# Kernel optimization log

Hardware: AMD Instinct MI355X
Metric: run time of the kernel (lower is better)

Reference implementation:

```python
import jax, jax.numpy as jnp
import numpy as np

N, E, HID, ED, L, H, D = 65536, 262144, 256, 64, 2, 8, 32
FF = 4 * HID
A_START = 8192  # first action gripper node; nodes [A_START:] are the T*K action nodes


def _ln(x, s, b, eps=1e-5):
    mu = jnp.mean(x, -1, keepdims=True)
    var = jnp.var(x, -1, keepdims=True)
    return (x - mu) * jax.lax.rsqrt(var + eps) * s + b


def _gnn_forward(x, edge_attr, edge_index, Wq, Wk, Wv, WeK, WeV, Wo,
                 ln1_s, ln1_b, ffn_w1, ffn_b1, ffn_w2, ffn_b2, ln2_s, ln2_b):
    # Hetero graph transformer over the single ('gripper','action','gripper') relation:
    # per-layer edge-indexed gather -> multi-head attention with edge features ->
    # segment softmax over incoming edges -> scatter-aggregate -> residual/LN/FFN.
    n = x.shape[0]
    e = edge_attr.shape[0]
    src, dst = edge_index[0], edge_index[1]
    inv_sqrt_d = np.float32(1.0 / np.sqrt(D))
    for l in range(Wq.shape[0]):
        q = (x @ Wq[l]).reshape(n, H, D)
        k = (x @ Wk[l]).reshape(n, H, D)
        v = (x @ Wv[l]).reshape(n, H, D)
        kj = k[src] + (edge_attr @ WeK[l]).reshape(e, H, D)  # [E,H,D] gathered keys + edge bias
        vj = v[src] + (edge_attr @ WeV[l]).reshape(e, H, D)
        score = jnp.einsum('ehd,ehd->eh', q[dst], kj) * inv_sqrt_d  # [E,H]
        smax = jax.ops.segment_max(score, dst, num_segments=n)
        p = jnp.exp(score - smax[dst])
        denom = jax.ops.segment_sum(p, dst, num_segments=n)
        alpha = p / denom[dst]  # segment softmax over incoming edges
        agg = jax.ops.segment_sum((alpha[..., None] * vj).reshape(e, H * D), dst, num_segments=n)
        x = _ln(x + agg @ Wo[l], ln1_s[l], ln1_b[l])
        hid = jax.nn.gelu(x @ ffn_w1[l] + ffn_b1[l], approximate=False) @ ffn_w2[l] + ffn_b2[l]
        x = _ln(x + hid, ln2_s[l], ln2_b[l])
    return x


def setup_inputs() -> dict:
    key = jax.random.key(0)
    ks = iter(jax.random.split(key, 16))
    w = lambda shape: jax.random.normal(next(ks), shape, jnp.float32) * 0.05
    return {
        "all_gripper_feats": jax.random.normal(next(ks), (N, HID), jnp.float32),
        "edge_attr": jax.random.normal(next(ks), (E, ED), jnp.float32),
        "Wq": w((L, HID, H * D)), "Wk": w((L, HID, H * D)), "Wv": w((L, HID, H * D)),
        "WeK": w((L, ED, H * D)), "WeV": w((L, ED, H * D)), "Wo": w((L, H * D, HID)),
        "ln1_s": jnp.ones((L, HID), jnp.float32), "ln1_b": jnp.zeros((L, HID), jnp.float32),
        "ffn_w1": w((L, HID, FF)), "ffn_b1": jnp.zeros((L, FF), jnp.float32),
        "ffn_w2": w((L, FF, HID)), "ffn_b2": jnp.zeros((L, HID), jnp.float32),
        "ln2_s": jnp.ones((L, HID), jnp.float32), "ln2_b": jnp.zeros((L, HID), jnp.float32),
        "head_w1": w((HID, HID)), "head_b1": jnp.zeros((HID,), jnp.float32),
        "head_w2": w((HID, 7)), "head_b2": jnp.zeros((7,), jnp.float32),
        "edge_index": jax.random.randint(next(ks), (2, E), 0, N),
        "action_start": A_START,
    }


def reference(all_gripper_feats, edge_attr, Wq, Wk, Wv, WeK, WeV, Wo,
              ln1_s, ln1_b, ffn_w1, ffn_b1, ffn_w2, ffn_b2, ln2_s, ln2_b,
              head_w1, head_b1, head_w2, head_b2, edge_index, action_start):
    x = _gnn_forward(all_gripper_feats, edge_attr, edge_index, Wq, Wk, Wv, WeK, WeV, Wo,
                     ln1_s, ln1_b, ffn_w1, ffn_b1, ffn_w2, ffn_b2, ln2_s, ln2_b)
    a = x[action_start:]  # action gripper nodes (T*K, hidden)
    return jax.nn.gelu(a @ head_w1 + head_b1, approximate=False) @ head_w2 + head_b2  # (T*K, 7)
```

## Files before the change

kernel.cpp:

```cpp
#include <hip/hip_runtime.h>
#include <hip/hip_bf16.h>
#include <math.h>

#define NN     65536
#define NE     262144
#define HIDN   256
#define EDIM   64
#define NHEAD  8
#define FFN    1024
#define ASTART 8192
#define NACT   (NN - ASTART)
#define NCH    32768
#define NCHUNK (NE / NCH)
#define DPC    (NN / NCHUNK)
#define RCH    32768

typedef __attribute__((ext_vector_type(8))) short short8;
typedef __attribute__((ext_vector_type(4))) short short4v;
typedef __attribute__((ext_vector_type(4))) float float4v;
typedef __hip_bfloat16 bf16;

__device__ __forceinline__ float b2f(short s) {
    union { unsigned u; float f; } c;
    c.u = ((unsigned)(unsigned short)s) << 16;
    return c.f;
}
__device__ __forceinline__ short f2b(float f) {
    __hip_bfloat16 h = __float2bfloat16(f);
    return *reinterpret_cast<short*>(&h);
}
__device__ __forceinline__ float gelu_exact(float v) {
    return 0.5f * v * (1.0f + erff(v * 0.70710678118654752f));
}
__device__ __forceinline__ void gload16(const void* g, void* l) {
    __builtin_amdgcn_global_load_lds(
        (const __attribute__((address_space(1))) void*)(uintptr_t)g,
        (__attribute__((address_space(3))) void*)(unsigned)(uintptr_t)l,
        16, 0, 0);
}

__global__ void convert_kernel(const float* __restrict__ src,
                               bf16* __restrict__ dst, int n) {
    int i = blockIdx.x * 256 + threadIdx.x;
    if (i < n) dst[i] = __float2bfloat16(src[i]);
}

__global__ void transpose_kernel(const float* __restrict__ src,
                                 bf16* __restrict__ dst, int R, int Cc) {
    int idx = blockIdx.x * 256 + threadIdx.x;
    if (idx >= R * Cc) return;
    int r = idx / Cc, c = idx - r * Cc;
    dst[(size_t)c * R + r] = __float2bfloat16(src[idx]);
}

__global__ void hist_kernel(const int* __restrict__ dstI, int* __restrict__ cnt) {
    int i = blockIdx.x * 256 + threadIdx.x;
    if (i < NE) atomicAdd(&cnt[dstI[i]], 1);
}
__global__ void scan1_kernel(const int* __restrict__ cnt, int* __restrict__ rp,
                             int* __restrict__ bsum) {
    __shared__ int s[256];
    int t = threadIdx.x, i = blockIdx.x * 256 + t;
    int v = cnt[i]; s[t] = v; __syncthreads();
    for (int off = 1; off < 256; off <<= 1) {
        int x = (t >= off) ? s[t - off] : 0; __syncthreads();
        s[t] += x; __syncthreads();
    }
    rp[i] = s[t] - v;
    if (t == 255) bsum[blockIdx.x] = s[255];
}
__global__ void scan2_kernel(int* __restrict__ bsum) {
    __shared__ int s[256];
    int t = threadIdx.x; int v = bsum[t]; s[t] = v; __syncthreads();
    for (int off = 1; off < 256; off <<= 1) {
        int x = (t >= off) ? s[t - off] : 0; __syncthreads();
        s[t] += x; __syncthreads();
    }
    bsum[t] = s[t] - v;
}
__global__ void scan3_kernel(int* __restrict__ rp, const int* __restrict__ bsum,
                             int* __restrict__ cursor) {
    int i = blockIdx.x * 256 + threadIdx.x;
    int v = rp[i] + bsum[i >> 8];
    rp[i] = v; cursor[i] = v;
    if (i == 0) rp[NN] = NE;
}
__global__ void scatter_kernel(const int* __restrict__ srcI, const int* __restrict__ dstI,
                               int* __restrict__ cursor, int* __restrict__ perm,
                               int* __restrict__ src_s, int* __restrict__ dst_s) {
    int e = blockIdx.x * 256 + threadIdx.x;
    if (e >= NE) return;
    int d = dstI[e];
    int pos = atomicAdd(&cursor[d], 1);
    perm[pos] = e; src_s[pos] = srcI[e]; dst_s[pos] = d;
}

template<int AMODE, bool DO_GELU>
__global__ __launch_bounds__(256) void gemm_kernel(
    const void* __restrict__ A,
    const bf16* __restrict__ BT,
    const bf16* __restrict__ bias,
    bf16* __restrict__ C,
    int M, int Nn, int K,
    const int* __restrict__ perm)
{
    __shared__ __align__(16) short As[2][128 * 32];
    __shared__ __align__(16) short Bs[2][128 * 32];

    const int t    = threadIdx.x;
    const int wave = t >> 6;
    const int lane = t & 63;
    const int l15  = lane & 15;
    const int quad = lane >> 4;
    const int wm   = (wave & 1) * 64;
    const int wn   = (wave >> 1) * 64;
    const int bm   = blockIdx.y * 128;
    const int bn   = blockIdx.x * 128;
    const int srow = t >> 2;
    const int sw   = srow & 3;
    const int scolB = ((t & 3) ^ sw) * 8;
    const int scolA = (t & 3) * 8;

    const short* Ab = (const short*)A  + (size_t)(bm + srow) * K + scolB;
    const short* Bb = (const short*)BT + (size_t)(bn + srow) * K + scolB;
    const float* Af0 = nullptr;
    const float* Af1 = nullptr;
    if (AMODE == 1) {
        Af0 = (const float*)A + (size_t)(bm + srow) * K + scolA;
        Af1 = Af0 + (size_t)64 * K;
    } else if (AMODE == 2) {
        const int pr0 = perm[bm + srow];
        const int pr1 = perm[bm + 64 + srow];
        Af0 = (const float*)A + (size_t)pr0 * K + scolA;
        Af1 = (const float*)A + (size_t)pr1 * K + scolA;
    }
    const int offW  = wave * 1024;
    const int offTs = (t * 16) ^ (sw << 4);
    const int qs16  = (quad ^ (l15 & 3)) * 16;

    float4v acc[4][4];
    #pragma unroll
    for (int i = 0; i < 4; ++i)
        #pragma unroll
        for (int j = 0; j < 4; ++j) acc[i][j] = (float4v){0.f, 0.f, 0.f, 0.f};

    const int nt = K >> 5;

    auto STAGE = [&](int b, int k0) {
        char* lA = (char*)As[b];
        char* lB = (char*)Bs[b];
        if (AMODE == 0) {
            gload16(Ab + k0,                  lA + offW);
            gload16(Ab + (size_t)64 * K + k0, lA + 4096 + offW);
        } else {
            #pragma unroll
            for (int i = 0; i < 2; ++i) {
                const float* s = (i ? Af1 : Af0) + k0;
                float4v f0 = *(const float4v*)s;
                float4v f1 = *(const float4v*)(s + 4);
                short8 w;
                #pragma unroll
                for (int j = 0; j < 4; ++j) { w[j] = f2b(f0[j]); w[4 + j] = f2b(f1[j]); }
                *(short8*)(lA + i * 4096 + offTs) = w;
            }
        }
        gload16(Bb + k0,                  lB + offW);
        gload16(Bb + (size_t)64 * K + k0, lB + 4096 + offW);
    };

    STAGE(0, 0);
    __syncthreads();

    for (int kt = 0; kt < nt; ++kt) {
        const int cur = kt & 1;
        if (kt + 1 < nt) STAGE(cur ^ 1, (kt + 1) * 32);

        const char* lA = (const char*)As[cur];
        const char* lB = (const char*)Bs[cur];
        short8 afr[4], bfr[4];
        #pragma unroll
        for (int i = 0; i < 4; ++i)
            afr[i] = *(const short8*)(lA + (wm + i * 16 + l15) * 64 + qs16);
        #pragma unroll
        for (int j = 0; j < 4; ++j)
            bfr[j] = *(const short8*)(lB + (wn + j * 16 + l15) * 64 + qs16);
        #pragma unroll
        for (int i = 0; i < 4; ++i)
            #pragma unroll
            for (int j = 0; j < 4; ++j)
                acc[i][j] = __builtin_amdgcn_mfma_f32_16x16x32_bf16(afr[i], bfr[j], acc[i][j], 0, 0, 0);
        __syncthreads();
    }

    #pragma unroll
    for (int j = 0; j < 4; ++j) {
        const int col = bn + wn + j * 16 + l15;
        const float bv = bias ? b2f(((const short*)bias)[col]) : 0.0f;
        #pragma unroll
        for (int i = 0; i < 4; ++i) {
            const int row0 = bm + wm + i * 16 + quad * 4;
            #pragma unroll
            for (int r = 0; r < 4; ++r) {
                float v = acc[i][j][r] + bv;
                if (DO_GELU) v = gelu_exact(v);
                C[(size_t)(row0 + r) * Nn + col] = __float2bfloat16(v);
            }
        }
    }
}

__global__ __launch_bounds__(256) void score_kernel(
    const bf16* __restrict__ q, const bf16* __restrict__ k,
    const bf16* __restrict__ eK,
    const int* __restrict__ src_s, const int* __restrict__ dst_s,
    short* __restrict__ pbuf, int e0, int qkstride)
{
    const int p = e0 + blockIdx.x * 4 + (threadIdx.x >> 6);
    const int lane = threadIdx.x & 63;
    const int s = src_s[p], d = dst_s[p];
    const int off = lane * 4;

    const short4v qv = *(const short4v*)((const short*)q  + (size_t)d * qkstride + off);
    const short4v kv = *(const short4v*)((const short*)k  + (size_t)s * qkstride + off);
    const short4v ev = *(const short4v*)((const short*)eK + (size_t)(p - e0) * HIDN + off);
    float x = 0.f;
    #pragma unroll
    for (int j = 0; j < 4; ++j) x += b2f(qv[j]) * (b2f(kv[j]) + b2f(ev[j]));
    x += __shfl_xor(x, 1);
    x += __shfl_xor(x, 2);
    x += __shfl_xor(x, 4);
    if ((lane & 7) == 0) {
        const float sc = fminf(fmaxf(x * 0.17677669529663689f, -30.f), 30.f);
        pbuf[(size_t)p * NHEAD + (lane >> 3)] = f2b(expf(sc));
    }
}

__global__ __launch_bounds__(256) void agg_kernel(
    const short* __restrict__ pbuf, const bf16* __restrict__ v,
    const bf16* __restrict__ eV,
    const int* __restrict__ src_s, const int* __restrict__ rp,
    float* __restrict__ agg, int e0, int e1, int dlo)
{
    const int d = dlo + blockIdx.x * 4 + (threadIdx.x >> 6);
    const int lane = threadIdx.x & 63;
    const int es = rp[d], ee = rp[d + 1];
    const int lo = es > e0 ? es : e0;
    const int hi = ee < e1 ? ee : e1;
    if (lo >= hi) return;
    const int h = lane >> 3, off = lane * 4;

    float den = 0.f;
    for (int p = es; p < ee; ++p) den += b2f(pbuf[(size_t)p * NHEAD + h]);

    float a0 = 0.f, a1 = 0.f, a2 = 0.f, a3 = 0.f;
    for (int p = lo; p < hi; ++p) {
        const float al = b2f(pbuf[(size_t)p * NHEAD + h]) / den;
        const int s = src_s[p];
        const short4v vv = *(const short4v*)((const short*)v  + (size_t)s * HIDN + off);
        const short4v ev = *(const short4v*)((const short*)eV + (size_t)(p - e0) * HIDN + off);
        a0 += al * (b2f(vv[0]) + b2f(ev[0]));
        a1 += al * (b2f(vv[1]) + b2f(ev[1]));
        a2 += al * (b2f(vv[2]) + b2f(ev[2]));
        a3 += al * (b2f(vv[3]) + b2f(ev[3]));
    }
    float* ao = agg + (size_t)d * HIDN + off;
    if (es >= e0 && ee <= e1) {
        *(float4v*)ao = (float4v){a0, a1, a2, a3};
    } else {
        atomicAdd(ao + 0, a0); atomicAdd(ao + 1, a1);
        atomicAdd(ao + 2, a2); atomicAdd(ao + 3, a3);
    }
}

__global__ __launch_bounds__(256) void ln_kernel(
    bf16* __restrict__ x, const bf16* __restrict__ t,
    const bf16* __restrict__ sc, const bf16* __restrict__ bi, int r0)
{
    const int row = r0 + blockIdx.x * 4 + (threadIdx.x >> 6);
    const int lane = threadIdx.x & 63;
    const size_t base = (size_t)row * HIDN + lane * 4;
    const size_t tbase = (size_t)(row - r0) * HIDN + lane * 4;
    const short4v xv = *(const short4v*)((const short*)x + base);
    const short4v tv = *(const short4v*)((const short*)t + tbase);
    float v[4];
    #pragma unroll
    for (int j = 0; j < 4; ++j) v[j] = b2f(xv[j]) + b2f(tv[j]);
    float sum = v[0] + v[1] + v[2] + v[3];
    float ssq = v[0]*v[0] + v[1]*v[1] + v[2]*v[2] + v[3]*v[3];
    #pragma unroll
    for (int m = 1; m < 64; m <<= 1) { sum += __shfl_xor(sum, m); ssq += __shfl_xor(ssq, m); }
    const float mean = sum * (1.0f / 256.0f);
    const float var  = fmaxf(ssq * (1.0f / 256.0f) - mean * mean, 0.0f);
    const float rstd = rsqrtf(var + 1e-5f);
    const short4v sv = *(const short4v*)((const short*)sc + lane * 4);
    const short4v bv = *(const short4v*)((const short*)bi + lane * 4);
    short4v out;
    #pragma unroll
    for (int j = 0; j < 4; ++j)
        out[j] = f2b((v[j] - mean) * rstd * b2f(sv[j]) + b2f(bv[j]));
    *(short4v*)((short*)x + base) = out;
}

__global__ __launch_bounds__(256) void head2_kernel(
    const bf16* __restrict__ h1, const bf16* __restrict__ w2T,
    const bf16* __restrict__ b2, float* __restrict__ out)
{
    const int row = blockIdx.x * 4 + (threadIdx.x >> 6);
    const int lane = threadIdx.x & 63;
    const int off = lane * 4;
    const short4v hv = *(const short4v*)((const short*)h1 + (size_t)row * HIDN + off);
    float hf[4];
    #pragma unroll
    for (int j = 0; j < 4; ++j) hf[j] = b2f(hv[j]);
    float acc[7];
    #pragma unroll
    for (int jc = 0; jc < 7; ++jc) {
        const short4v wv = *(const short4v*)((const short*)w2T + jc * HIDN + off);
        float a = hf[0]*b2f(wv[0]) + hf[1]*b2f(wv[1]) + hf[2]*b2f(wv[2]) + hf[3]*b2f(wv[3]);
        #pragma unroll
        for (int m = 1; m < 64; m <<= 1) a += __shfl_xor(a, m);
        acc[jc] = a;
    }
    if (lane < 7) {
        float r = lane == 0 ? acc[0] : lane == 1 ? acc[1] : lane == 2 ? acc[2] :
                  lane == 3 ? acc[3] : lane == 4 ? acc[4] : lane == 5 ? acc[5] : acc[6];
        out[(size_t)row * 7 + lane] = r + b2f(((const short*)b2)[lane]);
    }
}

extern "C" void kernel_launch(void* const* d_in, const int* in_sizes, int n_in,
                              void* d_out, int out_size, void* d_ws, size_t ws_size,
                              hipStream_t stream)
{
    const float* xin   = (const float*)d_in[0];
    const float* eattr = (const float*)d_in[1];
    const float* Wq    = (const float*)d_in[2];
    const float* Wk    = (const float*)d_in[3];
    const float* Wv    = (const float*)d_in[4];
    const float* WeK   = (const float*)d_in[5];
    const float* WeV   = (const float*)d_in[6];
    const float* Wo    = (const float*)d_in[7];
    const float* ln1s  = (const float*)d_in[8];
    const float* ln1b  = (const float*)d_in[9];
    const float* fw1   = (const float*)d_in[10];
    const float* fb1   = (const float*)d_in[11];
    const float* fw2   = (const float*)d_in[12];
    const float* fb2   = (const float*)d_in[13];
    const float* ln2s  = (const float*)d_in[14];
    const float* ln2b  = (const float*)d_in[15];
    const float* hw1   = (const float*)d_in[16];
    const float* hb1   = (const float*)d_in[17];
    const float* hw2   = (const float*)d_in[18];
    const float* hb2   = (const float*)d_in[19];
    const int*  eidx   = (const int*)d_in[20];
    const int*  srcI   = eidx;
    const int*  dstI   = eidx + NE;

    char* base = (char*)d_ws;
    size_t off = 0;
    auto carve = [&](size_t bytes) -> char* {
        char* p = base + off;
        off += (bytes + 255) & ~(size_t)255;
        return p;
    };
    bf16*  x_b    = (bf16*) carve((size_t)NN * HIDN * 2);
    bf16*  qk_b   = (bf16*) carve((size_t)NN * 2 * HIDN * 2);
    bf16*  v_b    = (bf16*) carve((size_t)NN * HIDN * 2);
    bf16*  echunk = (bf16*) carve((size_t)NCH * HIDN * 2);
    short* pbuf   = (short*)carve((size_t)NE * NHEAD * 2);
    int*   perm   = (int*)  carve((size_t)NE * 4);
    int*   src_s  = (int*)  carve((size_t)NE * 4);
    int*   dst_s  = (int*)  carve((size_t)NE * 4);
    int*   rowp   = (int*)  carve((size_t)(NN + 1) * 4);
    bf16*  WqkT   = (bf16*) carve((size_t)2 * HIDN * HIDN * 2);
    bf16*  WvT    = (bf16*) carve((size_t)HIDN * HIDN * 2);
    bf16*  WoT    = (bf16*) carve((size_t)HIDN * HIDN * 2);
    bf16*  WeKT   = (bf16*) carve((size_t)HIDN * EDIM * 2);
    bf16*  WeVT   = (bf16*) carve((size_t)HIDN * EDIM * 2);
    bf16*  W1T    = (bf16*) carve((size_t)FFN * HIDN * 2);
    bf16*  W2T    = (bf16*) carve((size_t)HIDN * FFN * 2);
    bf16*  HW1T   = (bf16*) carve((size_t)HIDN * HIDN * 2);
    bf16*  HW2T   = (bf16*) carve((size_t)8 * HIDN * 2);
    bf16*  c_ln1s = (bf16*) carve((size_t)2 * HIDN * 2);
    bf16*  c_ln1b = (bf16*) carve((size_t)2 * HIDN * 2);
    bf16*  c_ln2s = (bf16*) carve((size_t)2 * HIDN * 2);
    bf16*  c_ln2b = (bf16*) carve((size_t)2 * HIDN * 2);
    bf16*  c_fb1  = (bf16*) carve((size_t)2 * FFN * 2);
    bf16*  c_fb2  = (bf16*) carve((size_t)2 * HIDN * 2);
    bf16*  c_hb1  = (bf16*) carve((size_t)HIDN * 2);
    bf16*  c_hb2  = (bf16*) carve((size_t)16 * 2);
    if (off > ws_size) return;

    int* cnt    = (int*)echunk;
    int* cursor = cnt + NN;
    int* bsum   = cursor + NN;
    float* agg    = (float*)qk_b;
    bf16*  tmp_b  = v_b;
    bf16*  hid    = qk_b;
    bf16*  ffnout = v_b;

    const int TB = 256;
    #define GRID1(n) dim3(((n) + TB - 1) / TB)

    convert_kernel<<<GRID1(NN * HIDN), TB, 0, stream>>>(xin, x_b, NN * HIDN);
    convert_kernel<<<GRID1(2 * HIDN), TB, 0, stream>>>(ln1s, c_ln1s, 2 * HIDN);
    convert_kernel<<<GRID1(2 * HIDN), TB, 0, stream>>>(ln1b, c_ln1b, 2 * HIDN);
    convert_kernel<<<GRID1(2 * HIDN), TB, 0, stream>>>(ln2s, c_ln2s, 2 * HIDN);
    convert_kernel<<<GRID1(2 * HIDN), TB, 0, stream>>>(ln2b, c_ln2b, 2 * HIDN);
    convert_kernel<<<GRID1(2 * FFN), TB, 0, stream>>>(fb1, c_fb1, 2 * FFN);
    convert_kernel<<<GRID1(2 * HIDN), TB, 0, stream>>>(fb2, c_fb2, 2 * HIDN);
    convert_kernel<<<GRID1(HIDN), TB, 0, stream>>>(hb1, c_hb1, HIDN);
    convert_kernel<<<1, TB, 0, stream>>>(hb2, c_hb2, 7);
    transpose_kernel<<<GRID1(HIDN * HIDN), TB, 0, stream>>>(hw1, HW1T, HIDN, HIDN);
    transpose_kernel<<<GRID1(HIDN * 7), TB, 0, stream>>>(hw2, HW2T, HIDN, 7);

    hipMemsetAsync(cnt, 0, (size_t)NN * 4, stream);
    hist_kernel<<<GRID1(NE), TB, 0, stream>>>(dstI, cnt);
    scan1_kernel<<<NN / 256, 256, 0, stream>>>(cnt, rowp, bsum);
    scan2_kernel<<<1, 256, 0, stream>>>(bsum);
    scan3_kernel<<<NN / 256, 256, 0, stream>>>(rowp, bsum, cursor);
    scatter_kernel<<<GRID1(NE), TB, 0, stream>>>(srcI, dstI, cursor, perm, src_s, dst_s);

    for (int l = 0; l < 2; ++l) {
        transpose_kernel<<<GRID1(HIDN * HIDN), TB, 0, stream>>>(Wq + (size_t)l*HIDN*HIDN, WqkT, HIDN, HIDN);
        transpose_kernel<<<GRID1(HIDN * HIDN), TB, 0, stream>>>(Wk + (size_t)l*HIDN*HIDN, WqkT + (size_t)HIDN*HIDN, HIDN, HIDN);
        transpose_kernel<<<GRID1(HIDN * HIDN), TB, 0, stream>>>(Wv + (size_t)l*HIDN*HIDN, WvT, HIDN, HIDN);
        transpose_kernel<<<GRID1(EDIM * HIDN), TB, 0, stream>>>(WeK + (size_t)l*EDIM*HIDN, WeKT, EDIM, HIDN);
        transpose_kernel<<<GRID1(EDIM * HIDN), TB, 0, stream>>>(WeV + (size_t)l*EDIM*HIDN, WeVT, EDIM, HIDN);
        transpose_kernel<<<GRID1(HIDN * HIDN), TB, 0, stream>>>(Wo + (size_t)l*HIDN*HIDN, WoT, HIDN, HIDN);
        transpose_kernel<<<GRID1(HIDN * FFN),  TB, 0, stream>>>(fw1 + (size_t)l*HIDN*FFN, W1T, HIDN, FFN);
        transpose_kernel<<<GRID1(FFN * HIDN),  TB, 0, stream>>>(fw2 + (size_t)l*FFN*HIDN, W2T, FFN, HIDN);

        gemm_kernel<0, false><<<dim3((2*HIDN)/128, NN/128), TB, 0, stream>>>(x_b, WqkT, nullptr, qk_b, NN, 2*HIDN, HIDN, nullptr);
        gemm_kernel<0, false><<<dim3(HIDN/128, NN/128), TB, 0, stream>>>(x_b, WvT, nullptr, v_b, NN, HIDN, HIDN, nullptr);

        for (int c = 0; c < NCHUNK; ++c) {
            gemm_kernel<2, false><<<dim3(HIDN/128, NCH/128), TB, 0, stream>>>(
                eattr, WeKT, nullptr, echunk, NCH, HIDN, EDIM, perm + (size_t)c * NCH);
            score_kernel<<<NCH / 4, TB, 0, stream>>>(qk_b, qk_b + HIDN, echunk, src_s, dst_s, pbuf, c * NCH, 2 * HIDN);
        }

        hipMemsetAsync(agg, 0, (size_t)NN * HIDN * 4, stream);
        for (int c = 0; c < NCHUNK; ++c) {
            gemm_kernel<2, false><<<dim3(HIDN/128, NCH/128), TB, 0, stream>>>(
                eattr, WeVT, nullptr, echunk, NCH, HIDN, EDIM, perm + (size_t)c * NCH);
            const int dlo = (c == 0) ? 0 : (c - 1) * DPC;
            const int dhi = (c == NCHUNK - 1) ? NN : (c + 2) * DPC;
            agg_kernel<<<(dhi - dlo) / 4, TB, 0, stream>>>(
                pbuf, v_b, echunk, src_s, rowp, agg, c * NCH, (c + 1) * NCH, dlo);
        }

        gemm_kernel<1, false><<<dim3(HIDN/128, NN/128), TB, 0, stream>>>(agg, WoT, nullptr, tmp_b, NN, HIDN, HIDN, nullptr);
        ln_kernel<<<NN / 4, TB, 0, stream>>>(x_b, tmp_b, c_ln1s + (size_t)l * HIDN, c_ln1b + (size_t)l * HIDN, 0);

        for (int r0 = 0; r0 < NN; r0 += RCH) {
            gemm_kernel<0, true ><<<dim3(FFN/128, RCH/128), TB, 0, stream>>>(
                x_b + (size_t)r0 * HIDN, W1T, c_fb1 + (size_t)l * FFN, hid, RCH, FFN, HIDN, nullptr);
            gemm_kernel<0, false><<<dim3(HIDN/128, RCH/128), TB, 0, stream>>>(
                hid, W2T, c_fb2 + (size_t)l * HIDN, ffnout, RCH, HIDN, FFN, nullptr);
            ln_kernel<<<RCH / 4, TB, 0, stream>>>(x_b, ffnout, c_ln2s + (size_t)l * HIDN, c_ln2b + (size_t)l * HIDN, r0);
        }
    }

    gemm_kernel<0, true><<<dim3(HIDN/128, NACT/128), TB, 0, stream>>>(
        x_b + (size_t)ASTART * HIDN, HW1T, c_hb1, hid, NACT, HIDN, HIDN, nullptr);
    head2_kernel<<<NACT / 4, TB, 0, stream>>>(hid, HW2T, c_hb2, (float*)d_out);
}
```

Baseline: 1.704 ms.

## Approximate GELU, remap GEMM blocks across XCDs, vectorize input conversion

Three separate changes. The exact erff-based GELU in the GEMM epilogue becomes an Abramowitz-Stegun polynomial erf built on a hardware reciprocal and fast exp. The GEMM block index is remapped so neighbouring tiles land on the same XCD, for better L2 reuse. The large fp32-to-bf16 input conversion now handles four elements per thread with vector loads and stores. The erf approximation has about 1e-7 absolute error, which bf16 output hides, but it is a numeric change.

```diff
diff --git a/kernel.cpp b/kernel.cpp
--- a/kernel.cpp
+++ b/kernel.cpp
@@ -29,8 +29,16 @@
     __hip_bfloat16 h = __float2bfloat16(f);
     return *reinterpret_cast<short*>(&h);
 }
-__device__ __forceinline__ float gelu_exact(float v) {
-    return 0.5f * v * (1.0f + erff(v * 0.70710678118654752f));
+__device__ __forceinline__ float gelu_fast(float v) {
+    const float x  = v * 0.70710678118654752f;
+    const float ax = fabsf(x);
+    const float t  = __builtin_amdgcn_rcpf(1.0f + 0.3275911f * ax);
+    const float y  = t * (0.254829592f + t * (-0.284496736f + t * (1.421413741f +
+                     t * (-1.453152027f + t * 1.061405429f))));
+    const float e  = __expf(-x * x);
+    float erf = 1.0f - y * e;
+    erf = copysignf(erf, x);
+    return 0.5f * v * (1.0f + erf);
 }
 __device__ __forceinline__ void gload16(const void* g, void* l) {
     __builtin_amdgcn_global_load_lds(
@@ -43,6 +51,16 @@
                                bf16* __restrict__ dst, int n) {
     int i = blockIdx.x * 256 + threadIdx.x;
     if (i < n) dst[i] = __float2bfloat16(src[i]);
+}
+__global__ void convert4_kernel(const float* __restrict__ src,
+                                bf16* __restrict__ dst, int n4) {
+    int i = blockIdx.x * 256 + threadIdx.x;
+    if (i >= n4) return;
+    float4v f = *(const float4v*)(src + (size_t)i * 4);
+    short4v o;
+    #pragma unroll
+    for (int j = 0; j < 4; ++j) o[j] = f2b(f[j]);
+    *(short4v*)((short*)dst + (size_t)i * 4) = o;
 }
 
 __global__ void transpose_kernel(const float* __restrict__ src,
@@ -107,6 +125,15 @@
     __shared__ __align__(16) short As[2][128 * 32];
     __shared__ __align__(16) short Bs[2][128 * 32];
 
+    const int gx   = gridDim.x;
+    const int nwg  = gx * gridDim.y;
+    const int orig = blockIdx.y * gx + blockIdx.x;
+    const int q8   = nwg >> 3, r8 = nwg & 7;
+    const int xcd  = orig & 7, rk = orig >> 3;
+    const int nid  = (xcd < r8 ? xcd * (q8 + 1) : r8 * (q8 + 1) + (xcd - r8) * q8) + rk;
+    const int by   = nid / gx;
+    const int bx   = nid - by * gx;
+
     const int t    = threadIdx.x;
     const int wave = t >> 6;
     const int lane = t & 63;
@@ -114,8 +141,8 @@
     const int quad = lane >> 4;
     const int wm   = (wave & 1) * 64;
     const int wn   = (wave >> 1) * 64;
-    const int bm   = blockIdx.y * 128;
-    const int bn   = blockIdx.x * 128;
+    const int bm   = by * 128;
+    const int bn   = bx * 128;
     const int srow = t >> 2;
     const int sw   = srow & 3;
     const int scolB = ((t & 3) ^ sw) * 8;
@@ -202,7 +229,7 @@
             #pragma unroll
             for (int r = 0; r < 4; ++r) {
                 float v = acc[i][j][r] + bv;
-                if (DO_GELU) v = gelu_exact(v);
+                if (DO_GELU) v = gelu_fast(v);
                 C[(size_t)(row0 + r) * Nn + col] = __float2bfloat16(v);
             }
         }
@@ -402,7 +429,7 @@
     const int TB = 256;
     #define GRID1(n) dim3(((n) + TB - 1) / TB)
 
-    convert_kernel<<<GRID1(NN * HIDN), TB, 0, stream>>>(xin, x_b, NN * HIDN);
+    convert4_kernel<<<GRID1(NN * HIDN / 4), TB, 0, stream>>>(xin, x_b, NN * HIDN / 4);
     convert_kernel<<<GRID1(2 * HIDN), TB, 0, stream>>>(ln1s, c_ln1s, 2 * HIDN);
     convert_kernel<<<GRID1(2 * HIDN), TB, 0, stream>>>(ln1b, c_ln1b, 2 * HIDN);
     convert_kernel<<<GRID1(2 * HIDN), TB, 0, stream>>>(ln2s, c_ln2s, 2 * HIDN);
```

Measured after the change: 1.538 ms. 9.8% less time.
